# Kernel optimization log

Hardware: AMD Instinct MI355X
Metric: run time of the kernel (lower is better)

## Reference

```python
import jax, jax.numpy as jnp
import numpy as np

K = 5  # number of nearest neighbors (module default)


def setup_inputs() -> dict:
    key = jax.random.key(0)
    k1, k2 = jax.random.split(key)
    source_pc = jax.random.normal(k1, (2, 8192, 3), dtype=jnp.float32)
    target_pc = jax.random.normal(k2, (2, 8192, 3), dtype=jnp.float32)
    return {"source_pc": source_pc, "target_pc": target_pc}


def _valid_mask(pc_flat):
    # point is valid if any coordinate is nonzero (move_zero_point)
    return jnp.any(pc_flat != 0.0, axis=-1)


def reference(source_pc, target_pc):
    # move_zero_point flattens all batches into one batch-1 cloud; we emulate
    # the filtering with masks (invalid targets -> +inf distance, invalid
    # sources excluded from the mean) to stay jit-compatible.
    src = source_pc.reshape(-1, 3)   # [Ms, 3] query points
    tgt = target_pc.reshape(-1, 3)   # [Nt, 3] reference points
    src_mask = _valid_mask(src)      # [Ms]
    tgt_mask = _valid_mask(tgt)      # [Nt]

    # squared pairwise distances: |s|^2 + |t|^2 - 2 s.t  -> [Ms, Nt]
    s2 = jnp.sum(src * src, axis=-1)[:, None]
    t2 = jnp.sum(tgt * tgt, axis=-1)[None, :]
    d2 = s2 + t2 - 2.0 * jnp.einsum('md,nd->mn', src, tgt)
    d = jnp.sqrt(jnp.maximum(d2, 1e-12))

    BIG = jnp.float32(1e10)
    d = jnp.where(tgt_mask[None, :], d, BIG)  # drop zero target points

    # k smallest distances per source point (knn returns Euclidean dists)
    neg_topk, _ = jax.lax.top_k(-d, K)        # [Ms, K]
    knn_d = -neg_topk

    # mean over valid source points only
    w = src_mask.astype(knn_d.dtype)
    total = jnp.sum(knn_d * w[:, None])
    count = jnp.sum(w) * K
    return total / count
```

## Files before the change

kernel.cpp:

```cpp
#include <hip/hip_runtime.h>
#include <math.h>

#define KNN 5
#define BLOCK 256

#define G 28
#define NC (G * G * G)
#define NCPAD 24576
#define GRANGE 6.0f
#define H (2.0f * GRANGE / (float)G)
#define INVH ((float)G / (2.0f * GRANGE))
#define LPS 16

#define TILE_T 2048
#define WAVES_PER_BLOCK (BLOCK / 64)
#define SRCW 8
#define SRC_PER_BLOCK (WAVES_PER_BLOCK * SRCW)
#define NSPLIT 2

__device__ __forceinline__ float vmin(float a, float b) {
    float r;
    asm("v_min_f32 %0, %1, %2" : "=v"(r) : "v"(a), "v"(b));
    return r;
}
__device__ __forceinline__ float vmax(float a, float b) {
    float r;
    asm("v_max_f32 %0, %1, %2" : "=v"(r) : "v"(a), "v"(b));
    return r;
}

#define INS5(K0, K1, K2, K3, K4, V)                                       \
    do {                                                                  \
        float _v = (V);                                                   \
        K4 = __builtin_amdgcn_fmed3f(K3, K4, _v);                         \
        K3 = __builtin_amdgcn_fmed3f(K2, K3, _v);                         \
        K2 = __builtin_amdgcn_fmed3f(K1, K2, _v);                         \
        K1 = __builtin_amdgcn_fmed3f(K0, K1, _v);                         \
        K0 = vmin(K0, _v);                                                \
    } while (0)

#define MERGE55(a0, a1, a2, a3, a4, b0, b1, b2, b3, b4)                   \
    do {                                                                  \
        float r0 = vmin(a0, b0);                                          \
        float r1 = vmin(vmin(a1, b1), vmax(a0, b0));                      \
        float r2 = vmin(vmin(a2, b2), vmin(vmax(a0, b1), vmax(a1, b0)));  \
        float r3 = vmin(vmin(a3, b3),                                     \
                        vmin(vmax(a0, b2), vmin(vmax(a1, b1), vmax(a2, b0)))); \
        float r4 = vmin(vmin(a4, b4),                                     \
                        vmin(vmin(vmax(a0, b3), vmax(a1, b2)),            \
                             vmin(vmax(a2, b1), vmax(a3, b0))));          \
        a0 = r0; a1 = r1; a2 = r2; a3 = r3; a4 = r4;                      \
    } while (0)

__global__ void finalize_kernel(const float* acc, float* out) {
    out[0] = acc[0] / (acc[1] * (float)KNN);
}
__global__ void init_acc_kernel(float* acc) { acc[0] = 0.0f; acc[1] = 0.0f; }


__device__ __forceinline__ int cell_of(float x, float y, float z) {
    int cx = (int)floorf((x + GRANGE) * INVH);
    int cy = (int)floorf((y + GRANGE) * INVH);
    int cz = (int)floorf((z + GRANGE) * INVH);
    cx = min(max(cx, 0), G - 1);
    cy = min(max(cy, 0), G - 1);
    cz = min(max(cz, 0), G - 1);
    return (cz * G + cy) * G + cx;
}

__global__ void bin_count_kernel(const float* __restrict__ src,
                                 const float* __restrict__ tgt,
                                 int ms, int nt,
                                 int* __restrict__ cnt_s,
                                 int* __restrict__ cnt_t) {
    int i = blockIdx.x * blockDim.x + threadIdx.x;
    int n = ms + nt;
    for (; i < n; i += gridDim.x * blockDim.x) {
        bool isT = (i >= ms);
        const float* p = isT ? (tgt + 3 * (size_t)(i - ms)) : (src + 3 * (size_t)i);
        float x = p[0], y = p[1], z = p[2];
        if (isT && x == 0.0f && y == 0.0f && z == 0.0f) continue;
        atomicAdd((isT ? cnt_t : cnt_s) + cell_of(x, y, z), 1);
    }
}

__global__ __launch_bounds__(1024) void scan_kernel(int* ct, int* ot, int* cs, int* os) {
    __shared__ int psum[1024];
    int* c = blockIdx.x ? cs : ct;
    int* o = blockIdx.x ? os : ot;
    const int t = threadIdx.x;
    int4 v[6];
    const int4* c4 = reinterpret_cast<const int4*>(c) + t * 6;
#pragma unroll
    for (int j = 0; j < 6; ++j) v[j] = c4[j];
    int s = 0;
#pragma unroll
    for (int j = 0; j < 6; ++j) s += v[j].x + v[j].y + v[j].z + v[j].w;
    psum[t] = s;
    __syncthreads();
    for (int d = 1; d < 1024; d <<= 1) {
        int x = (t >= d) ? psum[t - d] : 0;
        __syncthreads();
        psum[t] += x;
        __syncthreads();
    }
    int run = t ? psum[t - 1] : 0;
    int4* o4 = reinterpret_cast<int4*>(o) + t * 6;
    int4* cc4 = reinterpret_cast<int4*>(c) + t * 6;
#pragma unroll
    for (int j = 0; j < 6; ++j) {
        int4 w;
        w.x = run; run += v[j].x;
        w.y = run; run += v[j].y;
        w.z = run; run += v[j].z;
        w.w = run; run += v[j].w;
        o4[j] = w;
        cc4[j] = w;
    }
    if (t == 1023) o[NCPAD] = run;
}

__global__ void scatter_kernel(const float* __restrict__ src,
                               const float* __restrict__ tgt,
                               int ms, int nt,
                               int* __restrict__ cur_s, int* __restrict__ cur_t,
                               float4* __restrict__ pts_s,
                               float4* __restrict__ pts_t) {
    int i = blockIdx.x * blockDim.x + threadIdx.x;
    int n = ms + nt;
    for (; i < n; i += gridDim.x * blockDim.x) {
        bool isT = (i >= ms);
        const float* p = isT ? (tgt + 3 * (size_t)(i - ms)) : (src + 3 * (size_t)i);
        float x = p[0], y = p[1], z = p[2];
        if (isT && x == 0.0f && y == 0.0f && z == 0.0f) continue;
        int cell = cell_of(x, y, z);
        int slot = atomicAdd((isT ? cur_t : cur_s) + cell, 1);
        float w = fmaf(x, x, fmaf(y, y, z * z));
        (isT ? pts_t : pts_s)[slot] = make_float4(x, y, z, w);
    }
}

__global__ __launch_bounds__(BLOCK) void knn_query_kernel(
        const float4* __restrict__ pts_s, const float4* __restrict__ pts_t,
        const int* __restrict__ off_t, float* __restrict__ acc,
        int* __restrict__ tail, int* __restrict__ tailcnt, int ms) {
    __shared__ float redS[4], redC[4];

    const int tid = threadIdx.x;
    const int g = tid >> 4;
    const int m = tid & 15;
    const int sidx = blockIdx.x * (BLOCK / LPS) + g;
    const bool live = (sidx < ms);

    float4 sp = pts_s[live ? sidx : 0];
    const float s2 = sp.w;
    const float nx = -2.0f * sp.x, ny = -2.0f * sp.y, nz = -2.0f * sp.z;

    int cx = (int)floorf((sp.x + GRANGE) * INVH);
    int cy = (int)floorf((sp.y + GRANGE) * INVH);
    int cz = (int)floorf((sp.z + GRANGE) * INVH);
    cx = min(max(cx, 0), G - 1);
    cy = min(max(cy, 0), G - 1);
    cz = min(max(cz, 0), G - 1);
    const int xlo = max(cx - 1, 0), xhi = min(cx + 1, G - 1);
    const float y0 = -GRANGE + cy * H, y1 = y0 + H;
    const float z0 = -GRANGE + cz * H, z1 = z0 + H;

    float q0 = 1e20f, q1 = 1e20f, q2 = 1e20f, q3 = 1e20f, q4 = 1e20f;

    {
        const int base = (cz * G + cy) * G;
        const int st = off_t[base + xlo];
        const int en = off_t[base + xhi + 1];
        for (int i = st + m; i < en; i += LPS) {
            float4 t = pts_t[i];
            float q = fmaf(nx, t.x, fmaf(ny, t.y, fmaf(nz, t.z, t.w)));
            INS5(q0, q1, q2, q3, q4, q);
        }
    }

    float lim;
    {
        float m0 = q0, m1 = q1, m2 = q2, m3 = q3, m4 = q4;
#pragma unroll
        for (int o = 8; o >= 1; o >>= 1) {
            float b0 = __shfl_xor(m0, o);
            float b1 = __shfl_xor(m1, o);
            float b2 = __shfl_xor(m2, o);
            float b3 = __shfl_xor(m3, o);
            float b4 = __shfl_xor(m4, o);
            MERGE55(m0, m1, m2, m3, m4, b0, b1, b2, b3, b4);
        }
        lim = m4 + s2;
    }

    const int DYA[8] = {-1, 1, 0, 0, -1, -1, 1, 1};
    const int DZA[8] = {0, 0, -1, 1, -1, 1, -1, 1};
#pragma unroll
    for (int r = 0; r < 8; ++r) {
        const int yy = cy + DYA[r], zz = cz + DZA[r];
        if ((unsigned)yy >= G || (unsigned)zz >= G) continue;
        float dys = (DYA[r] < 0) ? (sp.y - y0) : ((DYA[r] > 0) ? (y1 - sp.y) : 0.0f);
        float dzs = (DZA[r] < 0) ? (sp.z - z0) : ((DZA[r] > 0) ? (z1 - sp.z) : 0.0f);
        dys = fmaxf(dys, 0.0f);
        dzs = fmaxf(dzs, 0.0f);
        const float rb = fmaf(dys, dys, dzs * dzs);
        if (lim > rb) {
            const int base = (zz * G + yy) * G;
            const int st = off_t[base + xlo];
            const int en = off_t[base + xhi + 1];
            for (int i = st + m; i < en; i += LPS) {
                float4 t = pts_t[i];
                float q = fmaf(nx, t.x, fmaf(ny, t.y, fmaf(nz, t.z, t.w)));
                INS5(q0, q1, q2, q3, q4, q);
            }
        }
    }

#pragma unroll
    for (int o = 8; o >= 1; o >>= 1) {
        float b0 = __shfl_xor(q0, o);
        float b1 = __shfl_xor(q1, o);
        float b2 = __shfl_xor(q2, o);
        float b3 = __shfl_xor(q3, o);
        float b4 = __shfl_xor(q4, o);
        MERGE55(q0, q1, q2, q3, q4, b0, b1, b2, b3, b4);
    }

    float tsum = 0.0f, tcnt = 0.0f;
    if (live && m == 0) {
        const bool valid = (sp.x != 0.0f) || (sp.y != 0.0f) || (sp.z != 0.0f);
        if (valid) {
            const bool inbox = fabsf(sp.x) <= GRANGE && fabsf(sp.y) <= GRANGE &&
                               fabsf(sp.z) <= GRANGE;
            if (inbox && (q4 + s2 <= H * H)) {
                tsum = sqrtf(fmaxf(q0 + s2, 1e-12f)) + sqrtf(fmaxf(q1 + s2, 1e-12f)) +
                       sqrtf(fmaxf(q2 + s2, 1e-12f)) + sqrtf(fmaxf(q3 + s2, 1e-12f)) +
                       sqrtf(fmaxf(q4 + s2, 1e-12f));
                tcnt = 1.0f;
            } else {
                int ti = atomicAdd(tailcnt, 1);
                tail[ti] = sidx;
            }
        }
    }

#pragma unroll
    for (int off = 32; off >= 1; off >>= 1) {
        tsum += __shfl_down(tsum, off);
        tcnt += __shfl_down(tcnt, off);
    }
    const int wv = tid >> 6;
    if ((tid & 63) == 0) { redS[wv] = tsum; redC[wv] = tcnt; }
    __syncthreads();
    if (tid == 0) {
        float s = redS[0] + redS[1] + redS[2] + redS[3];
        float c = redC[0] + redC[1] + redC[2] + redC[3];
        if (s != 0.0f || c != 0.0f) {
            atomicAdd(&acc[0], s);
            atomicAdd(&acc[1], c);
        }
    }
}

__global__ __launch_bounds__(BLOCK) void knnB_kernel(
        const float4* __restrict__ pts_s, const float4* __restrict__ pts_t,
        const int* __restrict__ off_t, const int* __restrict__ tail,
        const int* __restrict__ tailcnt, float* __restrict__ acc) {
    __shared__ float bl[4][8];
    const int nv = off_t[NC];
    const int T = *tailcnt;
    const int tid = threadIdx.x;
    const int lane = tid & 63, wv = tid >> 6;
    float bsum = 0.0f, bcnt = 0.0f;

    for (int w = blockIdx.x; w < T; w += gridDim.x) {
        float4 sp = pts_s[tail[w]];
        const float s2 = sp.w;
        const float nx = -2.0f * sp.x, ny = -2.0f * sp.y, nz = -2.0f * sp.z;
        float q0 = 1e20f, q1 = 1e20f, q2 = 1e20f, q3 = 1e20f, q4 = 1e20f;
        for (int i = tid; i < nv; i += BLOCK) {
            float4 t = pts_t[i];
            float q = fmaf(nx, t.x, fmaf(ny, t.y, fmaf(nz, t.z, t.w)));
            INS5(q0, q1, q2, q3, q4, q);
        }
#pragma unroll
        for (int off = 32; off >= 1; off >>= 1) {
            float b0 = __shfl_xor(q0, off);
            float b1 = __shfl_xor(q1, off);
            float b2 = __shfl_xor(q2, off);
            float b3 = __shfl_xor(q3, off);
            float b4 = __shfl_xor(q4, off);
            MERGE55(q0, q1, q2, q3, q4, b0, b1, b2, b3, b4);
        }
        __syncthreads();
        if (lane == 0) {
            bl[wv][0] = q0; bl[wv][1] = q1; bl[wv][2] = q2;
            bl[wv][3] = q3; bl[wv][4] = q4;
        }
        __syncthreads();
        if (tid == 0) {
            float a0 = bl[0][0], a1 = bl[0][1], a2 = bl[0][2], a3 = bl[0][3],
                  a4 = bl[0][4];
#pragma unroll
            for (int k = 1; k < 4; ++k) {
                MERGE55(a0, a1, a2, a3, a4,
                        bl[k][0], bl[k][1], bl[k][2], bl[k][3], bl[k][4]);
            }
            bsum += sqrtf(fmaxf(a0 + s2, 1e-12f)) + sqrtf(fmaxf(a1 + s2, 1e-12f)) +
                    sqrtf(fmaxf(a2 + s2, 1e-12f)) + sqrtf(fmaxf(a3 + s2, 1e-12f)) +
                    sqrtf(fmaxf(a4 + s2, 1e-12f));
            bcnt += 1.0f;
        }
    }
    if (tid == 0 && blockIdx.x < T) {
        atomicAdd(&acc[0], bsum);
        atomicAdd(&acc[1], bcnt);
    }
}


__global__ __launch_bounds__(BLOCK, 4) void knn_split_kernel(
        const float* __restrict__ src, const float* __restrict__ tgt,
        float* __restrict__ partials, int ms, int nt, int nth, int spad) {
    __shared__ __align__(16) float xs[TILE_T];
    __shared__ __align__(16) float ys[TILE_T];
    __shared__ __align__(16) float zs[TILE_T];
    __shared__ __align__(16) float w2[TILE_T];

    const int tid = threadIdx.x;
    const int wv = tid >> 6;
    const int lane = tid & 63;
    const int sbase = (blockIdx.x * WAVES_PER_BLOCK + wv) * SRCW;
    const int half = blockIdx.y;
    const int hbase = half * nth;
    const int hend = min(nt, hbase + nth);

    float nx[SRCW], ny[SRCW], nz[SRCW];
#pragma unroll
    for (int s = 0; s < SRCW; ++s) {
        int sp = sbase + s;
        float x = 0.0f, y = 0.0f, z = 0.0f;
        if (sp < ms) {
            x = src[3 * sp + 0];
            y = src[3 * sp + 1];
            z = src[3 * sp + 2];
        }
        nx[s] = -2.0f * x; ny[s] = -2.0f * y; nz[s] = -2.0f * z;
    }
    float q0[SRCW], q1[SRCW], q2[SRCW], q3[SRCW], q4[SRCW];
#pragma unroll
    for (int s = 0; s < SRCW; ++s) {
        q0[s] = 1e30f; q1[s] = 1e30f; q2[s] = 1e30f; q3[s] = 1e30f; q4[s] = 1e30f;
    }

    for (int t0 = hbase; t0 < hend; t0 += TILE_T) {
        int cnt = min(TILE_T, hend - t0);
        for (int t = tid; t < TILE_T; t += BLOCK) {
            float x = 1e10f, y = 0.0f, z = 0.0f;
            if (t < cnt) {
                x = tgt[3 * (size_t)(t0 + t) + 0];
                y = tgt[3 * (size_t)(t0 + t) + 1];
                z = tgt[3 * (size_t)(t0 + t) + 2];
                if (x == 0.0f && y == 0.0f && z == 0.0f) { x = 1e10f; y = 0.0f; z = 0.0f; }
            }
            xs[t] = x; ys[t] = y; zs[t] = z;
            w2[t] = fmaf(x, x, fmaf(y, y, z * z));
        }
        __syncthreads();
#pragma unroll 2
        for (int i = 0; i < TILE_T / 256; ++i) {
            int t = (i << 8) + (lane << 2);
            float4 x4 = *reinterpret_cast<const float4*>(&xs[t]);
            float4 y4 = *reinterpret_cast<const float4*>(&ys[t]);
            float4 z4 = *reinterpret_cast<const float4*>(&zs[t]);
            float4 w4 = *reinterpret_cast<const float4*>(&w2[t]);
#pragma unroll
            for (int s = 0; s < SRCW; ++s) {
                float qa = fmaf(nx[s], x4.x, fmaf(ny[s], y4.x, fmaf(nz[s], z4.x, w4.x)));
                float qb = fmaf(nx[s], x4.y, fmaf(ny[s], y4.y, fmaf(nz[s], z4.y, w4.y)));
                float qc = fmaf(nx[s], x4.z, fmaf(ny[s], y4.z, fmaf(nz[s], z4.z, w4.z)));
                float qd = fmaf(nx[s], x4.w, fmaf(ny[s], y4.w, fmaf(nz[s], z4.w, w4.w)));
                INS5(q0[s], q1[s], q2[s], q3[s], q4[s], qa);
                INS5(q0[s], q1[s], q2[s], q3[s], q4[s], qb);
                INS5(q0[s], q1[s], q2[s], q3[s], q4[s], qc);
                INS5(q0[s], q1[s], q2[s], q3[s], q4[s], qd);
            }
        }
        __syncthreads();
    }
#pragma unroll
    for (int off = 32; off >= 1; off >>= 1) {
#pragma unroll
        for (int s = 0; s < SRCW; ++s) {
            float b0 = __shfl_xor(q0[s], off);
            float b1 = __shfl_xor(q1[s], off);
            float b2 = __shfl_xor(q2[s], off);
            float b3 = __shfl_xor(q3[s], off);
            float b4 = __shfl_xor(q4[s], off);
            MERGE55(q0[s], q1[s], q2[s], q3[s], q4[s], b0, b1, b2, b3, b4);
        }
    }
    if (lane == 0) {
        float* base = partials + ((size_t)half * spad + sbase) * 8;
#pragma unroll
        for (int s = 0; s < SRCW; ++s) {
            if (sbase + s < ms) {
                *reinterpret_cast<float4*>(base + 8 * s) =
                    make_float4(q0[s], q1[s], q2[s], q3[s]);
                *reinterpret_cast<float4*>(base + 8 * s + 4) =
                    make_float4(q4[s], 0.0f, 0.0f, 0.0f);
            }
        }
    }
}

__global__ __launch_bounds__(BLOCK) void merge_kernel(
        const float* __restrict__ src, const float* __restrict__ partials,
        float* __restrict__ acc, int ms, int spad) {
    __shared__ float red_s[WAVES_PER_BLOCK];
    __shared__ float red_c[WAVES_PER_BLOCK];
    const int tid = threadIdx.x;
    const int sp = blockIdx.x * BLOCK + tid;
    float ssum = 0.0f, scnt = 0.0f;
    if (sp < ms) {
        const float* r0p = partials + (size_t)sp * 8;
        const float* r1p = partials + ((size_t)spad + sp) * 8;
        float4 lo0 = *reinterpret_cast<const float4*>(r0p);
        float a4 = r0p[4];
        float4 lo1 = *reinterpret_cast<const float4*>(r1p);
        float b4 = r1p[4];
        float a0 = lo0.x, a1 = lo0.y, a2 = lo0.z, a3 = lo0.w;
        MERGE55(a0, a1, a2, a3, a4, lo1.x, lo1.y, lo1.z, lo1.w, b4);
        float x = src[3 * sp + 0];
        float y = src[3 * sp + 1];
        float z = src[3 * sp + 2];
        bool valid = (x != 0.0f) || (y != 0.0f) || (z != 0.0f);
        float s2 = fmaf(x, x, fmaf(y, y, z * z));
        if (valid) {
            ssum = sqrtf(fmaxf(a0 + s2, 1e-12f)) + sqrtf(fmaxf(a1 + s2, 1e-12f)) +
                   sqrtf(fmaxf(a2 + s2, 1e-12f)) + sqrtf(fmaxf(a3 + s2, 1e-12f)) +
                   sqrtf(fmaxf(a4 + s2, 1e-12f));
            scnt = 1.0f;
        }
    }
#pragma unroll
    for (int off = 32; off >= 1; off >>= 1) {
        ssum += __shfl_down(ssum, off);
        scnt += __shfl_down(scnt, off);
    }
    if ((tid & 63) == 0) { red_s[tid >> 6] = ssum; red_c[tid >> 6] = scnt; }
    __syncthreads();
    if (tid == 0) {
        float s = 0.0f, c = 0.0f;
#pragma unroll
        for (int i = 0; i < WAVES_PER_BLOCK; ++i) { s += red_s[i]; c += red_c[i]; }
        atomicAdd(&acc[0], s);
        atomicAdd(&acc[1], c);
    }
}


extern "C" void kernel_launch(void* const* d_in, const int* in_sizes, int n_in,
                              void* d_out, int out_size, void* d_ws, size_t ws_size,
                              hipStream_t stream) {
    const float* src = (const float*)d_in[0];
    const float* tgt = (const float*)d_in[1];
    const int ms = in_sizes[0] / 3;
    const int nt = in_sizes[1] / 3;

    char* p = (char*)d_ws;
    auto take = [&p](size_t bytes) {
        char* r = p;
        p += (bytes + 15) & ~(size_t)15;
        return r;
    };
    float* acc    = (float*)take(16);
    int* tailcnt  = (int*)(acc + 2);
    int* cnt_t    = (int*)take(NCPAD * sizeof(int));
    int* cnt_s    = (int*)take(NCPAD * sizeof(int));
    const size_t zero_bytes = (size_t)((char*)(cnt_s + NCPAD) - (char*)d_ws);
    int* off_t    = (int*)take((NCPAD + 1) * sizeof(int));
    int* off_s    = (int*)take((NCPAD + 1) * sizeof(int));
    float4* pts_t = (float4*)take((size_t)nt * sizeof(float4));
    float4* pts_s = (float4*)take((size_t)ms * sizeof(float4));
    int* tail     = (int*)take((size_t)ms * sizeof(int));
    const size_t need_grid = (size_t)(p - (char*)d_ws);

    if (ws_size >= need_grid) {
        const int n = ms + nt;
        hipMemsetAsync(d_ws, 0, zero_bytes, stream);
        bin_count_kernel<<<(n + 255) / 256, 256, 0, stream>>>(src, tgt, ms, nt,
                                                              cnt_s, cnt_t);
        scan_kernel<<<2, 1024, 0, stream>>>(cnt_t, off_t, cnt_s, off_s);
        scatter_kernel<<<(n + 255) / 256, 256, 0, stream>>>(src, tgt, ms, nt,
                                                            cnt_s, cnt_t, pts_s, pts_t);
        const int qblocks = (ms + (BLOCK / LPS) - 1) / (BLOCK / LPS);
        knn_query_kernel<<<qblocks, BLOCK, 0, stream>>>(pts_s, pts_t, off_t, acc,
                                                        tail, tailcnt, ms);
        knnB_kernel<<<1024, BLOCK, 0, stream>>>(pts_s, pts_t, off_t, tail,
                                                tailcnt, acc);
        finalize_kernel<<<1, 1, 0, stream>>>(acc, (float*)d_out);
        return;
    }

    float* acc2 = (float*)d_ws;
    init_acc_kernel<<<1, 1, 0, stream>>>(acc2);
    const int ngroups = (ms + SRC_PER_BLOCK - 1) / SRC_PER_BLOCK;
    const int spad = ngroups * SRC_PER_BLOCK;
    int nth = (nt + NSPLIT - 1) / NSPLIT;
    nth = (nth + TILE_T - 1) / TILE_T * TILE_T;
    float* partials = (float*)((char*)d_ws + 16);
    dim3 grid(ngroups, NSPLIT);
    knn_split_kernel<<<grid, BLOCK, 0, stream>>>(src, tgt, partials, ms, nt, nth, spad);
    merge_kernel<<<(ms + BLOCK - 1) / BLOCK, BLOCK, 0, stream>>>(src, partials,
                                                                 acc2, ms, spad);
    finalize_kernel<<<1, 1, 0, stream>>>(acc2, (float*)d_out);
}
```

Baseline: 96.35 us.

## Replace tail kernel with in-kernel ring search and fused last-block finalize

The query kernel now searches outward in shells of cells (radius up to 3) with box-distance pruning and stops early once the fifth-nearest distance lies inside the searched radius. Points that remain unresolved fall back to an in-kernel brute-force scan, which removes the separate tail kernel and tail list. Each lane keeps two interleaved top-5 lists to add ILP, source points are assigned to blocks in strided order to balance load, and the finalize step is folded into a last-block ticket. The cost is more divergence and more register pressure, and any fallback brute-force scan now runs at 16 lanes per query.

Result: slower. 182.4 us (+89.3%).

```diff
diff --git a/kernel.cpp b/kernel.cpp
--- a/kernel.cpp
+++ b/kernel.cpp
@@ -143,13 +143,14 @@
 __global__ __launch_bounds__(BLOCK) void knn_query_kernel(
         const float4* __restrict__ pts_s, const float4* __restrict__ pts_t,
         const int* __restrict__ off_t, float* __restrict__ acc,
-        int* __restrict__ tail, int* __restrict__ tailcnt, int ms) {
+        int* __restrict__ ticket, float* __restrict__ out, int ms) {
     __shared__ float redS[4], redC[4];
+    __shared__ int lastflag;
 
     const int tid = threadIdx.x;
     const int g = tid >> 4;
     const int m = tid & 15;
-    const int sidx = blockIdx.x * (BLOCK / LPS) + g;
+    const int sidx = g * gridDim.x + blockIdx.x;
     const bool live = (sidx < ms);
 
     float4 sp = pts_s[live ? sidx : 0];
@@ -162,86 +163,107 @@
     cx = min(max(cx, 0), G - 1);
     cy = min(max(cy, 0), G - 1);
     cz = min(max(cz, 0), G - 1);
-    const int xlo = max(cx - 1, 0), xhi = min(cx + 1, G - 1);
-    const float y0 = -GRANGE + cy * H, y1 = y0 + H;
-    const float z0 = -GRANGE + cz * H, z1 = z0 + H;
-
-    float q0 = 1e20f, q1 = 1e20f, q2 = 1e20f, q3 = 1e20f, q4 = 1e20f;
-
-    {
-        const int base = (cz * G + cy) * G;
-        const int st = off_t[base + xlo];
-        const int en = off_t[base + xhi + 1];
-        for (int i = st + m; i < en; i += LPS) {
-            float4 t = pts_t[i];
-            float q = fmaf(nx, t.x, fmaf(ny, t.y, fmaf(nz, t.z, t.w)));
-            INS5(q0, q1, q2, q3, q4, q);
-        }
-    }
-
-    float lim;
-    {
-        float m0 = q0, m1 = q1, m2 = q2, m3 = q3, m4 = q4;
+
+    float a0 = 1e20f, a1 = 1e20f, a2 = 1e20f, a3 = 1e20f, a4 = 1e20f;
+    float b0 = 1e20f, b1 = 1e20f, b2 = 1e20f, b3 = 1e20f, b4 = 1e20f;
+
+    auto scan_range = [&](int st, int en) {
+        for (int i = st + m; i < en; i += 2 * LPS) {
+            float4 t1 = pts_t[i];
+            int i2 = i + LPS;
+            bool h2 = (i2 < en);
+            float4 t2 = pts_t[h2 ? i2 : i];
+            float qa = fmaf(nx, t1.x, fmaf(ny, t1.y, fmaf(nz, t1.z, t1.w)));
+            float qb = h2 ? fmaf(nx, t2.x, fmaf(ny, t2.y, fmaf(nz, t2.z, t2.w)))
+                          : 1e20f;
+            INS5(a0, a1, a2, a3, a4, qa);
+            INS5(b0, b1, b2, b3, b4, qb);
+        }
+    };
+
+    auto scan_box = [&](int yy, int zz, int xa, int xb, float lim, bool prune) {
+        if ((unsigned)yy >= G || (unsigned)zz >= G) return;
+        xa = max(xa, 0);
+        xb = min(xb, G - 1);
+        if (xa > xb) return;
+        if (prune) {
+            float x0 = -GRANGE + xa * H, x1 = -GRANGE + (xb + 1) * H;
+            float y0 = -GRANGE + yy * H, y1 = y0 + H;
+            float z0 = -GRANGE + zz * H, z1 = z0 + H;
+            float dx = fmaxf(0.0f, fmaxf(x0 - sp.x, sp.x - x1));
+            float dy = fmaxf(0.0f, fmaxf(y0 - sp.y, sp.y - y1));
+            float dz = fmaxf(0.0f, fmaxf(z0 - sp.z, sp.z - z1));
+            float rb = fmaf(dx, dx, fmaf(dy, dy, dz * dz));
+            if (lim <= rb) return;
+        }
+        const int base = (zz * G + yy) * G;
+        scan_range(off_t[base + xa], off_t[base + xb + 1]);
+    };
+
+    auto merged_q4 = [&]() -> float {
+        float m0 = a0, m1 = a1, m2 = a2, m3 = a3, m4 = a4;
+        MERGE55(m0, m1, m2, m3, m4, b0, b1, b2, b3, b4);
 #pragma unroll
         for (int o = 8; o >= 1; o >>= 1) {
-            float b0 = __shfl_xor(m0, o);
-            float b1 = __shfl_xor(m1, o);
-            float b2 = __shfl_xor(m2, o);
-            float b3 = __shfl_xor(m3, o);
-            float b4 = __shfl_xor(m4, o);
-            MERGE55(m0, m1, m2, m3, m4, b0, b1, b2, b3, b4);
-        }
-        lim = m4 + s2;
-    }
-
-    const int DYA[8] = {-1, 1, 0, 0, -1, -1, 1, 1};
-    const int DZA[8] = {0, 0, -1, 1, -1, 1, -1, 1};
-#pragma unroll
-    for (int r = 0; r < 8; ++r) {
-        const int yy = cy + DYA[r], zz = cz + DZA[r];
-        if ((unsigned)yy >= G || (unsigned)zz >= G) continue;
-        float dys = (DYA[r] < 0) ? (sp.y - y0) : ((DYA[r] > 0) ? (y1 - sp.y) : 0.0f);
-        float dzs = (DZA[r] < 0) ? (sp.z - z0) : ((DZA[r] > 0) ? (z1 - sp.z) : 0.0f);
-        dys = fmaxf(dys, 0.0f);
-        dzs = fmaxf(dzs, 0.0f);
-        const float rb = fmaf(dys, dys, dzs * dzs);
-        if (lim > rb) {
-            const int base = (zz * G + yy) * G;
-            const int st = off_t[base + xlo];
-            const int en = off_t[base + xhi + 1];
-            for (int i = st + m; i < en; i += LPS) {
-                float4 t = pts_t[i];
-                float q = fmaf(nx, t.x, fmaf(ny, t.y, fmaf(nz, t.z, t.w)));
-                INS5(q0, q1, q2, q3, q4, q);
+            float c0 = __shfl_xor(m0, o);
+            float c1 = __shfl_xor(m1, o);
+            float c2 = __shfl_xor(m2, o);
+            float c3 = __shfl_xor(m3, o);
+            float c4 = __shfl_xor(m4, o);
+            MERGE55(m0, m1, m2, m3, m4, c0, c1, c2, c3, c4);
+        }
+        return m4;
+    };
+
+    scan_box(cy, cz, cx, cx, 0.0f, false);
+    float lim = merged_q4() + s2;
+    bool done = false;
+    for (int r = 1; r <= 3 && !done; ++r) {
+        for (int dz = -r; dz <= r; ++dz) {
+            for (int dy = -r; dy <= r; ++dy) {
+                const int yy = cy + dy, zz = cz + dz;
+                const bool perim = (dz == -r || dz == r || dy == -r || dy == r);
+                if (perim) {
+                    scan_box(yy, zz, cx - r, cx + r, lim, true);
+                } else {
+                    scan_box(yy, zz, cx - r, cx - r, lim, true);
+                    scan_box(yy, zz, cx + r, cx + r, lim, true);
+                }
             }
         }
-    }
-
+        lim = merged_q4() + s2;
+        const float rh = (float)r * H;
+        done = (lim <= rh * rh);
+    }
+
+    const bool inbox = fabsf(sp.x) <= GRANGE && fabsf(sp.y) <= GRANGE &&
+                       fabsf(sp.z) <= GRANGE;
+    if (!done || !inbox) {
+        a0 = a1 = a2 = a3 = a4 = 1e20f;
+        b0 = b1 = b2 = b3 = b4 = 1e20f;
+        const int nv = off_t[NC];
+        scan_range(0, nv);
+    }
+
+    MERGE55(a0, a1, a2, a3, a4, b0, b1, b2, b3, b4);
 #pragma unroll
     for (int o = 8; o >= 1; o >>= 1) {
-        float b0 = __shfl_xor(q0, o);
-        float b1 = __shfl_xor(q1, o);
-        float b2 = __shfl_xor(q2, o);
-        float b3 = __shfl_xor(q3, o);
-        float b4 = __shfl_xor(q4, o);
-        MERGE55(q0, q1, q2, q3, q4, b0, b1, b2, b3, b4);
+        float c0 = __shfl_xor(a0, o);
+        float c1 = __shfl_xor(a1, o);
+        float c2 = __shfl_xor(a2, o);
+        float c3 = __shfl_xor(a3, o);
+        float c4 = __shfl_xor(a4, o);
+        MERGE55(a0, a1, a2, a3, a4, c0, c1, c2, c3, c4);
     }
 
     float tsum = 0.0f, tcnt = 0.0f;
     if (live && m == 0) {
         const bool valid = (sp.x != 0.0f) || (sp.y != 0.0f) || (sp.z != 0.0f);
         if (valid) {
-            const bool inbox = fabsf(sp.x) <= GRANGE && fabsf(sp.y) <= GRANGE &&
-                               fabsf(sp.z) <= GRANGE;
-            if (inbox && (q4 + s2 <= H * H)) {
-                tsum = sqrtf(fmaxf(q0 + s2, 1e-12f)) + sqrtf(fmaxf(q1 + s2, 1e-12f)) +
-                       sqrtf(fmaxf(q2 + s2, 1e-12f)) + sqrtf(fmaxf(q3 + s2, 1e-12f)) +
-                       sqrtf(fmaxf(q4 + s2, 1e-12f));
-                tcnt = 1.0f;
-            } else {
-                int ti = atomicAdd(tailcnt, 1);
-                tail[ti] = sidx;
-            }
+            tsum = sqrtf(fmaxf(a0 + s2, 1e-12f)) + sqrtf(fmaxf(a1 + s2, 1e-12f)) +
+                   sqrtf(fmaxf(a2 + s2, 1e-12f)) + sqrtf(fmaxf(a3 + s2, 1e-12f)) +
+                   sqrtf(fmaxf(a4 + s2, 1e-12f));
+            tcnt = 1.0f;
         }
     }
 
@@ -256,66 +278,17 @@
     if (tid == 0) {
         float s = redS[0] + redS[1] + redS[2] + redS[3];
         float c = redC[0] + redC[1] + redC[2] + redC[3];
-        if (s != 0.0f || c != 0.0f) {
-            atomicAdd(&acc[0], s);
-            atomicAdd(&acc[1], c);
-        }
-    }
-}
-
-__global__ __launch_bounds__(BLOCK) void knnB_kernel(
-        const float4* __restrict__ pts_s, const float4* __restrict__ pts_t,
-        const int* __restrict__ off_t, const int* __restrict__ tail,
-        const int* __restrict__ tailcnt, float* __restrict__ acc) {
-    __shared__ float bl[4][8];
-    const int nv = off_t[NC];
-    const int T = *tailcnt;
-    const int tid = threadIdx.x;
-    const int lane = tid & 63, wv = tid >> 6;
-    float bsum = 0.0f, bcnt = 0.0f;
-
-    for (int w = blockIdx.x; w < T; w += gridDim.x) {
-        float4 sp = pts_s[tail[w]];
-        const float s2 = sp.w;
-        const float nx = -2.0f * sp.x, ny = -2.0f * sp.y, nz = -2.0f * sp.z;
-        float q0 = 1e20f, q1 = 1e20f, q2 = 1e20f, q3 = 1e20f, q4 = 1e20f;
-        for (int i = tid; i < nv; i += BLOCK) {
-            float4 t = pts_t[i];
-            float q = fmaf(nx, t.x, fmaf(ny, t.y, fmaf(nz, t.z, t.w)));
-            INS5(q0, q1, q2, q3, q4, q);
-        }
-#pragma unroll
-        for (int off = 32; off >= 1; off >>= 1) {
-            float b0 = __shfl_xor(q0, off);
-            float b1 = __shfl_xor(q1, off);
-            float b2 = __shfl_xor(q2, off);
-            float b3 = __shfl_xor(q3, off);
-            float b4 = __shfl_xor(q4, off);
-            MERGE55(q0, q1, q2, q3, q4, b0, b1, b2, b3, b4);
-        }
-        __syncthreads();
-        if (lane == 0) {
-            bl[wv][0] = q0; bl[wv][1] = q1; bl[wv][2] = q2;
-            bl[wv][3] = q3; bl[wv][4] = q4;
-        }
-        __syncthreads();
-        if (tid == 0) {
-            float a0 = bl[0][0], a1 = bl[0][1], a2 = bl[0][2], a3 = bl[0][3],
-                  a4 = bl[0][4];
-#pragma unroll
-            for (int k = 1; k < 4; ++k) {
-                MERGE55(a0, a1, a2, a3, a4,
-                        bl[k][0], bl[k][1], bl[k][2], bl[k][3], bl[k][4]);
-            }
-            bsum += sqrtf(fmaxf(a0 + s2, 1e-12f)) + sqrtf(fmaxf(a1 + s2, 1e-12f)) +
-                    sqrtf(fmaxf(a2 + s2, 1e-12f)) + sqrtf(fmaxf(a3 + s2, 1e-12f)) +
-                    sqrtf(fmaxf(a4 + s2, 1e-12f));
-            bcnt += 1.0f;
-        }
-    }
-    if (tid == 0 && blockIdx.x < T) {
-        atomicAdd(&acc[0], bsum);
-        atomicAdd(&acc[1], bcnt);
+        atomicAdd(&acc[0], s);
+        atomicAdd(&acc[1], c);
+        __threadfence();
+        int t = atomicAdd(ticket, 1);
+        lastflag = (t == (int)gridDim.x - 1) ? 1 : 0;
+    }
+    __syncthreads();
+    if (tid == 0 && lastflag) {
+        float ss = atomicAdd(&acc[0], 0.0f);
+        float cc = atomicAdd(&acc[1], 0.0f);
+        out[0] = ss / (cc * (float)KNN);
     }
 }
 
@@ -476,7 +449,7 @@
         return r;
     };
     float* acc    = (float*)take(16);
-    int* tailcnt  = (int*)(acc + 2);
+    int* ticket   = (int*)(acc + 2);
     int* cnt_t    = (int*)take(NCPAD * sizeof(int));
     int* cnt_s    = (int*)take(NCPAD * sizeof(int));
     const size_t zero_bytes = (size_t)((char*)(cnt_s + NCPAD) - (char*)d_ws);
@@ -484,7 +457,6 @@
     int* off_s    = (int*)take((NCPAD + 1) * sizeof(int));
     float4* pts_t = (float4*)take((size_t)nt * sizeof(float4));
     float4* pts_s = (float4*)take((size_t)ms * sizeof(float4));
-    int* tail     = (int*)take((size_t)ms * sizeof(int));
     const size_t need_grid = (size_t)(p - (char*)d_ws);
 
     if (ws_size >= need_grid) {
@@ -497,10 +469,7 @@
                                                             cnt_s, cnt_t, pts_s, pts_t);
         const int qblocks = (ms + (BLOCK / LPS) - 1) / (BLOCK / LPS);
         knn_query_kernel<<<qblocks, BLOCK, 0, stream>>>(pts_s, pts_t, off_t, acc,
-                                                        tail, tailcnt, ms);
-        knnB_kernel<<<1024, BLOCK, 0, stream>>>(pts_s, pts_t, off_t, tail,
-                                                tailcnt, acc);
-        finalize_kernel<<<1, 1, 0, stream>>>(acc, (float*)d_out);
+                                                        ticket, (float*)d_out, ms);
         return;
     }
 
```

## Grid-stride query kernel, dual-accumulator scans, prefetched row offsets, fused finalize

Applied to the files above, without the earlier changes.

The query kernel now runs a fixed grid of 512 blocks that stride over chunks of 16 sources, instead of one block per chunk. It loads all nine row offsets and bounds up front and scans each range with two independent top-5 accumulators per lane, which adds memory-level parallelism and ILP. The last-block ticket pattern in knnB folds in the final division, so the separate finalize launch goes away. The trade-offs are more registers from the doubled accumulators and prefetched arrays, and an extra atomic and fence per block.

New measurement: 98.51 us. 1.02x slower.

```diff
diff --git a/kernel.cpp b/kernel.cpp
--- a/kernel.cpp
+++ b/kernel.cpp
@@ -11,6 +11,8 @@
 #define H (2.0f * GRANGE / (float)G)
 #define INVH ((float)G / (2.0f * GRANGE))
 #define LPS 16
+#define SPC (BLOCK / LPS)
+#define QBLOCKS 512
 
 #define TILE_T 2048
 #define WAVES_PER_BLOCK (BLOCK / 64)
@@ -143,104 +145,117 @@
 __global__ __launch_bounds__(BLOCK) void knn_query_kernel(
         const float4* __restrict__ pts_s, const float4* __restrict__ pts_t,
         const int* __restrict__ off_t, float* __restrict__ acc,
-        int* __restrict__ tail, int* __restrict__ tailcnt, int ms) {
+        int* __restrict__ tail, int* __restrict__ tailcnt, int ms, int nchunk) {
     __shared__ float redS[4], redC[4];
 
     const int tid = threadIdx.x;
     const int g = tid >> 4;
     const int m = tid & 15;
-    const int sidx = blockIdx.x * (BLOCK / LPS) + g;
-    const bool live = (sidx < ms);
-
-    float4 sp = pts_s[live ? sidx : 0];
-    const float s2 = sp.w;
-    const float nx = -2.0f * sp.x, ny = -2.0f * sp.y, nz = -2.0f * sp.z;
-
-    int cx = (int)floorf((sp.x + GRANGE) * INVH);
-    int cy = (int)floorf((sp.y + GRANGE) * INVH);
-    int cz = (int)floorf((sp.z + GRANGE) * INVH);
-    cx = min(max(cx, 0), G - 1);
-    cy = min(max(cy, 0), G - 1);
-    cz = min(max(cz, 0), G - 1);
-    const int xlo = max(cx - 1, 0), xhi = min(cx + 1, G - 1);
-    const float y0 = -GRANGE + cy * H, y1 = y0 + H;
-    const float z0 = -GRANGE + cz * H, z1 = z0 + H;
-
-    float q0 = 1e20f, q1 = 1e20f, q2 = 1e20f, q3 = 1e20f, q4 = 1e20f;
-
-    {
-        const int base = (cz * G + cy) * G;
-        const int st = off_t[base + xlo];
-        const int en = off_t[base + xhi + 1];
-        for (int i = st + m; i < en; i += LPS) {
-            float4 t = pts_t[i];
-            float q = fmaf(nx, t.x, fmaf(ny, t.y, fmaf(nz, t.z, t.w)));
-            INS5(q0, q1, q2, q3, q4, q);
-        }
-    }
-
-    float lim;
-    {
-        float m0 = q0, m1 = q1, m2 = q2, m3 = q3, m4 = q4;
+    float tsum = 0.0f, tcnt = 0.0f;
+
+    for (int c = blockIdx.x; c < nchunk; c += gridDim.x) {
+        const int sidx = c * SPC + g;
+        const bool live = (sidx < ms);
+
+        float4 sp = pts_s[live ? sidx : 0];
+        const float s2 = sp.w;
+        const float nx = -2.0f * sp.x, ny = -2.0f * sp.y, nz = -2.0f * sp.z;
+
+        int cx = (int)floorf((sp.x + GRANGE) * INVH);
+        int cy = (int)floorf((sp.y + GRANGE) * INVH);
+        int cz = (int)floorf((sp.z + GRANGE) * INVH);
+        cx = min(max(cx, 0), G - 1);
+        cy = min(max(cy, 0), G - 1);
+        cz = min(max(cz, 0), G - 1);
+        const int xlo = max(cx - 1, 0), xhi = min(cx + 1, G - 1);
+        const float y0 = -GRANGE + cy * H, y1 = y0 + H;
+        const float z0 = -GRANGE + cz * H, z1 = z0 + H;
+
+        const int DY[9] = {0, -1, 1, 0, 0, -1, -1, 1, 1};
+        const int DZ[9] = {0, 0, 0, -1, 1, -1, 1, -1, 1};
+        int rst[9], ren[9];
+        float rb[9];
+#pragma unroll
+        for (int r = 0; r < 9; ++r) {
+            const int yy = cy + DY[r], zz = cz + DZ[r];
+            const bool ok = ((unsigned)yy < G) && ((unsigned)zz < G);
+            const int base = (zz * G + yy) * G;
+            rst[r] = ok ? off_t[base + xlo] : 0;
+            ren[r] = ok ? off_t[base + xhi + 1] : 0;
+            float dys = (DY[r] < 0) ? (sp.y - y0) : ((DY[r] > 0) ? (y1 - sp.y) : 0.0f);
+            float dzs = (DZ[r] < 0) ? (sp.z - z0) : ((DZ[r] > 0) ? (z1 - sp.z) : 0.0f);
+            dys = fmaxf(dys, 0.0f);
+            dzs = fmaxf(dzs, 0.0f);
+            rb[r] = fmaf(dys, dys, dzs * dzs);
+        }
+
+        float a0 = 1e20f, a1 = 1e20f, a2 = 1e20f, a3 = 1e20f, a4 = 1e20f;
+        float b0 = 1e20f, b1 = 1e20f, b2 = 1e20f, b3 = 1e20f, b4 = 1e20f;
+
+        auto scan_range = [&](int st, int en) {
+            for (int i = st + m; i < en; i += 2 * LPS) {
+                float4 t1 = pts_t[i];
+                int i2 = i + LPS;
+                bool h2 = (i2 < en);
+                float4 t2 = pts_t[h2 ? i2 : i];
+                float qa = fmaf(nx, t1.x, fmaf(ny, t1.y, fmaf(nz, t1.z, t1.w)));
+                float qb = h2 ? fmaf(nx, t2.x, fmaf(ny, t2.y, fmaf(nz, t2.z, t2.w)))
+                              : 1e20f;
+                INS5(a0, a1, a2, a3, a4, qa);
+                INS5(b0, b1, b2, b3, b4, qb);
+            }
+        };
+
+        scan_range(rst[0], ren[0]);
+
+        float lim;
+        {
+            float m0 = a0, m1 = a1, m2 = a2, m3 = a3, m4 = a4;
+            MERGE55(m0, m1, m2, m3, m4, b0, b1, b2, b3, b4);
+#pragma unroll
+            for (int o = 8; o >= 1; o >>= 1) {
+                float c0 = __shfl_xor(m0, o);
+                float c1 = __shfl_xor(m1, o);
+                float c2 = __shfl_xor(m2, o);
+                float c3 = __shfl_xor(m3, o);
+                float c4 = __shfl_xor(m4, o);
+                MERGE55(m0, m1, m2, m3, m4, c0, c1, c2, c3, c4);
+            }
+            lim = m4 + s2;
+        }
+
+#pragma unroll
+        for (int r = 1; r < 9; ++r) {
+            if (lim > rb[r]) scan_range(rst[r], ren[r]);
+        }
+
+        MERGE55(a0, a1, a2, a3, a4, b0, b1, b2, b3, b4);
 #pragma unroll
         for (int o = 8; o >= 1; o >>= 1) {
-            float b0 = __shfl_xor(m0, o);
-            float b1 = __shfl_xor(m1, o);
-            float b2 = __shfl_xor(m2, o);
-            float b3 = __shfl_xor(m3, o);
-            float b4 = __shfl_xor(m4, o);
-            MERGE55(m0, m1, m2, m3, m4, b0, b1, b2, b3, b4);
-        }
-        lim = m4 + s2;
-    }
-
-    const int DYA[8] = {-1, 1, 0, 0, -1, -1, 1, 1};
-    const int DZA[8] = {0, 0, -1, 1, -1, 1, -1, 1};
-#pragma unroll
-    for (int r = 0; r < 8; ++r) {
-        const int yy = cy + DYA[r], zz = cz + DZA[r];
-        if ((unsigned)yy >= G || (unsigned)zz >= G) continue;
-        float dys = (DYA[r] < 0) ? (sp.y - y0) : ((DYA[r] > 0) ? (y1 - sp.y) : 0.0f);
-        float dzs = (DZA[r] < 0) ? (sp.z - z0) : ((DZA[r] > 0) ? (z1 - sp.z) : 0.0f);
-        dys = fmaxf(dys, 0.0f);
-        dzs = fmaxf(dzs, 0.0f);
-        const float rb = fmaf(dys, dys, dzs * dzs);
-        if (lim > rb) {
-            const int base = (zz * G + yy) * G;
-            const int st = off_t[base + xlo];
-            const int en = off_t[base + xhi + 1];
-            for (int i = st + m; i < en; i += LPS) {
-                float4 t = pts_t[i];
-                float q = fmaf(nx, t.x, fmaf(ny, t.y, fmaf(nz, t.z, t.w)));
-                INS5(q0, q1, q2, q3, q4, q);
-            }
-        }
-    }
-
-#pragma unroll
-    for (int o = 8; o >= 1; o >>= 1) {
-        float b0 = __shfl_xor(q0, o);
-        float b1 = __shfl_xor(q1, o);
-        float b2 = __shfl_xor(q2, o);
-        float b3 = __shfl_xor(q3, o);
-        float b4 = __shfl_xor(q4, o);
-        MERGE55(q0, q1, q2, q3, q4, b0, b1, b2, b3, b4);
-    }
-
-    float tsum = 0.0f, tcnt = 0.0f;
-    if (live && m == 0) {
-        const bool valid = (sp.x != 0.0f) || (sp.y != 0.0f) || (sp.z != 0.0f);
-        if (valid) {
-            const bool inbox = fabsf(sp.x) <= GRANGE && fabsf(sp.y) <= GRANGE &&
-                               fabsf(sp.z) <= GRANGE;
-            if (inbox && (q4 + s2 <= H * H)) {
-                tsum = sqrtf(fmaxf(q0 + s2, 1e-12f)) + sqrtf(fmaxf(q1 + s2, 1e-12f)) +
-                       sqrtf(fmaxf(q2 + s2, 1e-12f)) + sqrtf(fmaxf(q3 + s2, 1e-12f)) +
-                       sqrtf(fmaxf(q4 + s2, 1e-12f));
-                tcnt = 1.0f;
-            } else {
-                int ti = atomicAdd(tailcnt, 1);
-                tail[ti] = sidx;
+            float c0 = __shfl_xor(a0, o);
+            float c1 = __shfl_xor(a1, o);
+            float c2 = __shfl_xor(a2, o);
+            float c3 = __shfl_xor(a3, o);
+            float c4 = __shfl_xor(a4, o);
+            MERGE55(a0, a1, a2, a3, a4, c0, c1, c2, c3, c4);
+        }
+
+        if (live && m == 0) {
+            const bool valid = (sp.x != 0.0f) || (sp.y != 0.0f) || (sp.z != 0.0f);
+            if (valid) {
+                const bool inbox = fabsf(sp.x) <= GRANGE &&
+                                   fabsf(sp.y) <= GRANGE && fabsf(sp.z) <= GRANGE;
+                if (inbox && (a4 + s2 <= H * H)) {
+                    tsum += sqrtf(fmaxf(a0 + s2, 1e-12f)) +
+                            sqrtf(fmaxf(a1 + s2, 1e-12f)) +
+                            sqrtf(fmaxf(a2 + s2, 1e-12f)) +
+                            sqrtf(fmaxf(a3 + s2, 1e-12f)) +
+                            sqrtf(fmaxf(a4 + s2, 1e-12f));
+                    tcnt += 1.0f;
+                } else {
+                    int ti = atomicAdd(tailcnt, 1);
+                    tail[ti] = sidx;
+                }
             }
         }
     }
@@ -266,7 +281,8 @@
 __global__ __launch_bounds__(BLOCK) void knnB_kernel(
         const float4* __restrict__ pts_s, const float4* __restrict__ pts_t,
         const int* __restrict__ off_t, const int* __restrict__ tail,
-        const int* __restrict__ tailcnt, float* __restrict__ acc) {
+        const int* __restrict__ tailcnt, float* __restrict__ acc,
+        int* __restrict__ ticket, float* __restrict__ out) {
     __shared__ float bl[4][8];
     const int nv = off_t[NC];
     const int T = *tailcnt;
@@ -313,9 +329,19 @@
             bcnt += 1.0f;
         }
     }
-    if (tid == 0 && blockIdx.x < T) {
-        atomicAdd(&acc[0], bsum);
-        atomicAdd(&acc[1], bcnt);
+
+    if (tid == 0) {
+        if (bcnt != 0.0f) {
+            atomicAdd(&acc[0], bsum);
+            atomicAdd(&acc[1], bcnt);
+        }
+        __threadfence();
+        int t = atomicAdd(ticket, 1);
+        if (t == (int)gridDim.x - 1) {
+            float ss = atomicAdd(&acc[0], 0.0f);
+            float cc = atomicAdd(&acc[1], 0.0f);
+            out[0] = ss / (cc * (float)KNN);
+        }
     }
 }
 
@@ -476,7 +502,8 @@
         return r;
     };
     float* acc    = (float*)take(16);
-    int* tailcnt  = (int*)(acc + 2);
+    int* ticket   = (int*)(acc + 2);
+    int* tailcnt  = (int*)(acc + 3);
     int* cnt_t    = (int*)take(NCPAD * sizeof(int));
     int* cnt_s    = (int*)take(NCPAD * sizeof(int));
     const size_t zero_bytes = (size_t)((char*)(cnt_s + NCPAD) - (char*)d_ws);
@@ -495,12 +522,12 @@
         scan_kernel<<<2, 1024, 0, stream>>>(cnt_t, off_t, cnt_s, off_s);
         scatter_kernel<<<(n + 255) / 256, 256, 0, stream>>>(src, tgt, ms, nt,
                                                             cnt_s, cnt_t, pts_s, pts_t);
-        const int qblocks = (ms + (BLOCK / LPS) - 1) / (BLOCK / LPS);
-        knn_query_kernel<<<qblocks, BLOCK, 0, stream>>>(pts_s, pts_t, off_t, acc,
-                                                        tail, tailcnt, ms);
+        const int nchunk = (ms + SPC - 1) / SPC;
+        knn_query_kernel<<<QBLOCKS, BLOCK, 0, stream>>>(pts_s, pts_t, off_t, acc,
+                                                        tail, tailcnt, ms, nchunk);
         knnB_kernel<<<1024, BLOCK, 0, stream>>>(pts_s, pts_t, off_t, tail,
-                                                tailcnt, acc);
-        finalize_kernel<<<1, 1, 0, stream>>>(acc, (float*)d_out);
+                                                tailcnt, acc, ticket,
+                                                (float*)d_out);
         return;
     }
 
```
